# Kernel tuning notes

Hardware: AMD Instinct MI355X
Metric: run time of the kernel (lower is better)

## Reference

```python
import jax, jax.numpy as jnp
import numpy as np

T, N = 512, 256          # timesteps, parallel envs
STATE, HID = 64, 128     # input features, GRU hidden size


def setup_inputs() -> dict:
    key = jax.random.key(0)
    k = jax.random.split(key, 6)
    inputs = jax.random.normal(k[0], (T * N, STATE), dtype=jnp.float32)
    hxs = jax.random.normal(k[1], (N, HID), dtype=jnp.float32)
    masks = (jax.random.uniform(k[2], (T * N, 1)) > 0.02).astype(jnp.float32)
    # GRU params (torch layout: gates ordered r, z, n; rows = 3*HID)
    weight_ih = jax.random.normal(k[3], (3 * HID, STATE), dtype=jnp.float32) * 0.1
    weight_hh = jax.random.normal(k[4], (3 * HID, HID), dtype=jnp.float32) * 0.1
    bias_ih = jnp.zeros((3 * HID,), dtype=jnp.float32)  # init.constant_(0)
    bias_hh = jnp.zeros((3 * HID,), dtype=jnp.float32)
    return {
        "inputs": inputs, "hxs": hxs, "masks": masks,
        "weight_ih": weight_ih, "weight_hh": weight_hh,
        "bias_ih": bias_ih, "bias_hh": bias_hh,
    }


def reference(inputs, hxs, masks, weight_ih, weight_hh, bias_ih, bias_hh):
    n, hid = hxs.shape
    t = inputs.shape[0] // n
    x = inputs.reshape(t, n, -1)       # (t, n, state)
    m = masks.reshape(t, n, 1)         # (t, n, 1)

    # Input-to-gate projections are mask-independent: precompute for all steps.
    gx = jnp.einsum('tns,gs->tng', x, weight_ih) + bias_ih  # (t, n, 3H)

    def step(h, xs):
        gx_t, m_t = xs
        h = h * m_t                                 # inline reset (fused; replaces chunk splitting)
        gh = h @ weight_hh.T + bias_hh              # (n, 3H)
        xr, xz, xn = jnp.split(gx_t, 3, axis=-1)
        hr, hz, hn = jnp.split(gh, 3, axis=-1)
        r = jax.nn.sigmoid(xr + hr)
        z = jax.nn.sigmoid(xz + hz)
        cand = jnp.tanh(xn + r * hn)
        h = (1.0 - z) * cand + z * h                # torch GRU update
        return h, h

    h_final, ys = jax.lax.scan(step, hxs, (gx, m))  # ys: (t, n, H)
    return ys.reshape(t * n, hid), h_final
```

## Files before the change

kernel.cpp:

```cpp
#include <hip/hip_runtime.h>
#include <math.h>

#define T_STEPS  512
#define N_ENVS   256
#define STATE    64
#define HID      128
#define NTHREADS 512
#define XPAD     72

typedef _Float16 half8   __attribute__((ext_vector_type(8)));
typedef _Float16 half4_t __attribute__((ext_vector_type(4)));
typedef float    floatx4 __attribute__((ext_vector_type(4)));

__global__ __launch_bounds__(NTHREADS, 2) void gru_r6(
    const float* __restrict__ x,
    const float* __restrict__ h0,
    const float* __restrict__ masks,
    const float* __restrict__ wih,
    const float* __restrict__ whh,
    const float* __restrict__ bih,
    const float* __restrict__ bhh,
    float* __restrict__ out)
{
    const int b    = blockIdx.x;
    const int tid  = threadIdx.x;
    const int w    = tid >> 6;
    const int lane = tid & 63;
    const int c    = lane & 15;
    const int quad = lane >> 4;
    const int j    = 16 * w + c;

    __shared__ __align__(16) _Float16 buf[2][HID];
    __shared__ __align__(16) _Float16 xh[2][16][XPAD];
    __shared__ __align__(16) _Float16 gxp[16][HID][4];

    const int rowb[3] = { j, HID + j, 2 * HID + j };
    half8 Bh[3][4];
#pragma unroll
    for (int ti = 0; ti < 3; ++ti) {
        const int g = rowb[ti];
#pragma unroll
        for (int kt = 0; kt < 4; ++kt) {
            const float* src = whh + (size_t)g * HID + kt * 32 + quad * 8;
            const float4 p0 = *(const float4*)(src);
            const float4 p1 = *(const float4*)(src + 4);
            half8 hb;
            hb[0] = (_Float16)p0.x; hb[1] = (_Float16)p0.y;
            hb[2] = (_Float16)p0.z; hb[3] = (_Float16)p0.w;
            hb[4] = (_Float16)p1.x; hb[5] = (_Float16)p1.y;
            hb[6] = (_Float16)p1.z; hb[7] = (_Float16)p1.w;
            Bh[ti][kt] = hb;
        }
    }
    half8 Bx[3][2];
#pragma unroll
    for (int ti = 0; ti < 3; ++ti) {
        const int g = rowb[ti];
#pragma unroll
        for (int kt = 0; kt < 2; ++kt) {
            const float* src = wih + (size_t)g * STATE + kt * 32 + quad * 8;
            const float4 p0 = *(const float4*)(src);
            const float4 p1 = *(const float4*)(src + 4);
            half8 hb;
            hb[0] = (_Float16)p0.x; hb[1] = (_Float16)p0.y;
            hb[2] = (_Float16)p0.z; hb[3] = (_Float16)p0.w;
            hb[4] = (_Float16)p1.x; hb[5] = (_Float16)p1.y;
            hb[6] = (_Float16)p1.z; hb[7] = (_Float16)p1.w;
            Bx[ti][kt] = hb;
        }
    }

    const float br  = bih[j] + bhh[j];
    const float bz  = bih[HID + j] + bhh[HID + j];
    const float bxn = bih[2 * HID + j];
    const float bhn = bhh[2 * HID + j];

    float hr = h0[(size_t)b * HID + j];
    float hm = masks[b] * hr;
    if (quad == 0) buf[0][j] = (_Float16)hm;

    float4 xp = {0.f, 0.f, 0.f, 0.f};
    if (tid < 256) {
        const int k = tid >> 4, cc = (tid & 15) * 4;
        const float4 xv = *(const float4*)(x + ((size_t)k * N_ENVS + b) * STATE + cc);
        half4_t hx = {(_Float16)xv.x, (_Float16)xv.y, (_Float16)xv.z, (_Float16)xv.w};
        *(half4_t*)&xh[0][k][cc] = hx;
        xp = *(const float4*)(x + ((size_t)(16 + k) * N_ENVS + b) * STATE + cc);
    }
    float mwin  = masks[(size_t)(1  + (lane & 15)) * N_ENVS + b];
    float mwin_nxt = masks[(size_t)(17 + (lane & 15)) * N_ENVS + b];

    float o[4] = {0.f, 0.f, 0.f, 0.f};

    __syncthreads();

    const floatx4 zero4 = {0.f, 0.f, 0.f, 0.f};

    for (int tc = 0; tc < 32; ++tc) {
        if (tc > 0) {
            const int tbp = (tc - 1) * 16;
#pragma unroll
            for (int i = 0; i < 4; ++i)
                out[((size_t)(tbp + quad * 4 + i) * N_ENVS + b) * HID + j] = o[i];
            mwin = mwin_nxt;
            const int stm = (tc + 1) * 16 + 1 + (lane & 15);
            mwin_nxt = masks[(size_t)(stm < T_STEPS ? stm : T_STEPS - 1) * N_ENVS + b];
        }
        if (tid < 256) {
            const int k = tid >> 4, cc = (tid & 15) * 4;
            half4_t hx = {(_Float16)xp.x, (_Float16)xp.y, (_Float16)xp.z, (_Float16)xp.w};
            *(half4_t*)&xh[(tc + 1) & 1][k][cc] = hx;
            const int st = (tc + 2) * 16 + k;
            if (st < T_STEPS)
                xp = *(const float4*)(x + ((size_t)st * N_ENVS + b) * STATE + cc);
        }

        {
            const _Float16* xr = &xh[tc & 1][c][0];
            half8 ax0 = *(const half8*)&xr[quad * 8];
            half8 ax1 = *(const half8*)&xr[32 + quad * 8];
            floatx4 g0 = __builtin_amdgcn_mfma_f32_16x16x32_f16(ax0, Bx[0][0], zero4, 0, 0, 0);
            floatx4 g1 = __builtin_amdgcn_mfma_f32_16x16x32_f16(ax0, Bx[1][0], zero4, 0, 0, 0);
            floatx4 g2 = __builtin_amdgcn_mfma_f32_16x16x32_f16(ax0, Bx[2][0], zero4, 0, 0, 0);
            g0 = __builtin_amdgcn_mfma_f32_16x16x32_f16(ax1, Bx[0][1], g0, 0, 0, 0);
            g1 = __builtin_amdgcn_mfma_f32_16x16x32_f16(ax1, Bx[1][1], g1, 0, 0, 0);
            g2 = __builtin_amdgcn_mfma_f32_16x16x32_f16(ax1, Bx[2][1], g2, 0, 0, 0);
#pragma unroll
            for (int i = 0; i < 4; ++i) {
                half4_t p;
                p[0] = (_Float16)(g0[i] + br);
                p[1] = (_Float16)(g1[i] + bz);
                p[2] = (_Float16)(g2[i] + bxn);
                p[3] = (_Float16)0.f;
                *(half4_t*)&gxp[quad * 4 + i][j][0] = p;
            }
        }
        __syncthreads();

#pragma unroll
        for (int s = 0; s < 16; ++s) {
            const int t = tc * 16 + s;
            const _Float16* bufc = buf[s & 1];
            _Float16* bufn = (_Float16*)buf[(s + 1) & 1];

            half8 a0 = *(const half8*)(bufc + 0 * 32 + quad * 8);
            half8 a1 = *(const half8*)(bufc + 1 * 32 + quad * 8);
            half8 a2 = *(const half8*)(bufc + 2 * 32 + quad * 8);
            half8 a3 = *(const half8*)(bufc + 3 * 32 + quad * 8);
            const half4_t gxh = *(const half4_t*)&gxp[s][j][0];

            floatx4 r_a = __builtin_amdgcn_mfma_f32_16x16x32_f16(a0, Bh[0][0], zero4, 0, 0, 0);
            floatx4 r_b = __builtin_amdgcn_mfma_f32_16x16x32_f16(a2, Bh[0][2], zero4, 0, 0, 0);
            floatx4 z_a = __builtin_amdgcn_mfma_f32_16x16x32_f16(a0, Bh[1][0], zero4, 0, 0, 0);
            floatx4 z_b = __builtin_amdgcn_mfma_f32_16x16x32_f16(a2, Bh[1][2], zero4, 0, 0, 0);
            floatx4 n_a = __builtin_amdgcn_mfma_f32_16x16x32_f16(a0, Bh[2][0], zero4, 0, 0, 0);
            floatx4 n_b = __builtin_amdgcn_mfma_f32_16x16x32_f16(a2, Bh[2][2], zero4, 0, 0, 0);
            r_a = __builtin_amdgcn_mfma_f32_16x16x32_f16(a1, Bh[0][1], r_a, 0, 0, 0);
            r_b = __builtin_amdgcn_mfma_f32_16x16x32_f16(a3, Bh[0][3], r_b, 0, 0, 0);
            z_a = __builtin_amdgcn_mfma_f32_16x16x32_f16(a1, Bh[1][1], z_a, 0, 0, 0);
            z_b = __builtin_amdgcn_mfma_f32_16x16x32_f16(a3, Bh[1][3], z_b, 0, 0, 0);
            n_a = __builtin_amdgcn_mfma_f32_16x16x32_f16(a1, Bh[2][1], n_a, 0, 0, 0);
            n_b = __builtin_amdgcn_mfma_f32_16x16x32_f16(a3, Bh[2][3], n_b, 0, 0, 0);

            const float ur = (r_a[0] + r_b[0]) + (float)gxh[0];
            const float uz = (z_a[0] + z_b[0]) + (float)gxh[1];
            const float hn = (n_a[0] + n_b[0]) + bhn;
            const float xn = (float)gxh[2];

            const float e_r = __expf(-ur);
            const float r   = __builtin_amdgcn_rcpf(1.f + e_r);
            const float a   = fmaf(r, hn, xn);
            const float e_t = __expf(-2.f * fabsf(a));
            const float e_z = __expf(-fmaxf(uz, -30.f));
            const float opt = 1.f + e_t;
            float num = copysignf(e_z * (1.f - e_t), a);
            num = fmaf(hm, opt, num);
            const float den = opt * (1.f + e_z);
            const float hnew = num * __builtin_amdgcn_rcpf(den);

            o[s & 3] = (quad == (s >> 2)) ? hnew : o[s & 3];

            if (t < T_STEPS - 1) {
                const int   mi = __builtin_amdgcn_readlane(__float_as_int(mwin), s);
                const float mn = __int_as_float(mi);
                hm = mn * hnew;
                if (quad == 0) bufn[j] = (_Float16)hm;
            }
            hr = hnew;
            __syncthreads();
        }
    }

    {
        const int tbp = 31 * 16;
#pragma unroll
        for (int i = 0; i < 4; ++i)
            out[((size_t)(tbp + quad * 4 + i) * N_ENVS + b) * HID + j] = o[i];
    }
    if (quad == 0)
        out[(size_t)T_STEPS * N_ENVS * HID + (size_t)b * HID + j] = hr;
}

extern "C" void kernel_launch(void* const* d_in, const int* in_sizes, int n_in,
                              void* d_out, int out_size, void* d_ws, size_t ws_size,
                              hipStream_t stream) {
    const float* x   = (const float*)d_in[0];
    const float* h0  = (const float*)d_in[1];
    const float* mk  = (const float*)d_in[2];
    const float* wih = (const float*)d_in[3];
    const float* whh = (const float*)d_in[4];
    const float* bih = (const float*)d_in[5];
    const float* bhh = (const float*)d_in[6];
    float* out = (float*)d_out;

    hipLaunchKernelGGL(gru_r6, dim3(N_ENVS), dim3(NTHREADS), 0, stream,
                       x, h0, mk, wih, whh, bih, bhh, out);
}
```

Measured before the change: 291.9 us.

## Fold exp2 scaling into GRU weights, use raw v_exp and lighter barriers

```diff
diff --git a/kernel.cpp b/kernel.cpp
--- a/kernel.cpp
+++ b/kernel.cpp
@@ -12,7 +12,15 @@
 typedef _Float16 half4_t __attribute__((ext_vector_type(4)));
 typedef float    floatx4 __attribute__((ext_vector_type(4)));
 
-__global__ __launch_bounds__(NTHREADS, 2) void gru_r6(
+#define BAR() asm volatile("s_waitcnt lgkmcnt(0)\n\ts_barrier" ::: "memory")
+
+__device__ __forceinline__ float fexp2(float v) {
+    float r;
+    asm("v_exp_f32 %0, %1" : "=v"(r) : "v"(v));
+    return r;
+}
+
+__global__ __launch_bounds__(NTHREADS, 2) void gru_r7(
     const float* __restrict__ x,
     const float* __restrict__ h0,
     const float* __restrict__ masks,
@@ -32,23 +40,28 @@
 
     __shared__ __align__(16) _Float16 buf[2][HID];
     __shared__ __align__(16) _Float16 xh[2][16][XPAD];
-    __shared__ __align__(16) _Float16 gxp[16][HID][4];
+    __shared__ __align__(16) float    gxp[16][HID][4];
+
+    const float SRZ = -1.44269504088896341f;
+    const float SN  = -2.88539008177792681f;
+    const float scl[3] = { SRZ, SRZ, SN };
 
     const int rowb[3] = { j, HID + j, 2 * HID + j };
     half8 Bh[3][4];
 #pragma unroll
     for (int ti = 0; ti < 3; ++ti) {
         const int g = rowb[ti];
+        const float sc = scl[ti];
 #pragma unroll
         for (int kt = 0; kt < 4; ++kt) {
             const float* src = whh + (size_t)g * HID + kt * 32 + quad * 8;
             const float4 p0 = *(const float4*)(src);
             const float4 p1 = *(const float4*)(src + 4);
             half8 hb;
-            hb[0] = (_Float16)p0.x; hb[1] = (_Float16)p0.y;
-            hb[2] = (_Float16)p0.z; hb[3] = (_Float16)p0.w;
-            hb[4] = (_Float16)p1.x; hb[5] = (_Float16)p1.y;
-            hb[6] = (_Float16)p1.z; hb[7] = (_Float16)p1.w;
+            hb[0] = (_Float16)(sc * p0.x); hb[1] = (_Float16)(sc * p0.y);
+            hb[2] = (_Float16)(sc * p0.z); hb[3] = (_Float16)(sc * p0.w);
+            hb[4] = (_Float16)(sc * p1.x); hb[5] = (_Float16)(sc * p1.y);
+            hb[6] = (_Float16)(sc * p1.z); hb[7] = (_Float16)(sc * p1.w);
             Bh[ti][kt] = hb;
         }
     }
@@ -56,24 +69,25 @@
 #pragma unroll
     for (int ti = 0; ti < 3; ++ti) {
         const int g = rowb[ti];
+        const float sc = scl[ti];
 #pragma unroll
         for (int kt = 0; kt < 2; ++kt) {
             const float* src = wih + (size_t)g * STATE + kt * 32 + quad * 8;
             const float4 p0 = *(const float4*)(src);
             const float4 p1 = *(const float4*)(src + 4);
             half8 hb;
-            hb[0] = (_Float16)p0.x; hb[1] = (_Float16)p0.y;
-            hb[2] = (_Float16)p0.z; hb[3] = (_Float16)p0.w;
-            hb[4] = (_Float16)p1.x; hb[5] = (_Float16)p1.y;
-            hb[6] = (_Float16)p1.z; hb[7] = (_Float16)p1.w;
+            hb[0] = (_Float16)(sc * p0.x); hb[1] = (_Float16)(sc * p0.y);
+            hb[2] = (_Float16)(sc * p0.z); hb[3] = (_Float16)(sc * p0.w);
+            hb[4] = (_Float16)(sc * p1.x); hb[5] = (_Float16)(sc * p1.y);
+            hb[6] = (_Float16)(sc * p1.z); hb[7] = (_Float16)(sc * p1.w);
             Bx[ti][kt] = hb;
         }
     }
 
-    const float br  = bih[j] + bhh[j];
-    const float bz  = bih[HID + j] + bhh[HID + j];
-    const float bxn = bih[2 * HID + j];
-    const float bhn = bhh[2 * HID + j];
+    const float br  = SRZ * (bih[j] + bhh[j]);
+    const float bz  = SRZ * (bih[HID + j] + bhh[HID + j]);
+    const float bxn = SN  * bih[2 * HID + j];
+    const float bhn = SN  * bhh[2 * HID + j];
 
     float hr = h0[(size_t)b * HID + j];
     float hm = masks[b] * hr;
@@ -87,12 +101,12 @@
         *(half4_t*)&xh[0][k][cc] = hx;
         xp = *(const float4*)(x + ((size_t)(16 + k) * N_ENVS + b) * STATE + cc);
     }
-    float mwin  = masks[(size_t)(1  + (lane & 15)) * N_ENVS + b];
+    float mwin     = masks[(size_t)(1  + (lane & 15)) * N_ENVS + b];
     float mwin_nxt = masks[(size_t)(17 + (lane & 15)) * N_ENVS + b];
 
     float o[4] = {0.f, 0.f, 0.f, 0.f};
 
-    __syncthreads();
+    BAR();
 
     const floatx4 zero4 = {0.f, 0.f, 0.f, 0.f};
 
@@ -127,27 +141,27 @@
             g2 = __builtin_amdgcn_mfma_f32_16x16x32_f16(ax1, Bx[2][1], g2, 0, 0, 0);
 #pragma unroll
             for (int i = 0; i < 4; ++i) {
-                half4_t p;
-                p[0] = (_Float16)(g0[i] + br);
-                p[1] = (_Float16)(g1[i] + bz);
-                p[2] = (_Float16)(g2[i] + bxn);
-                p[3] = (_Float16)0.f;
-                *(half4_t*)&gxp[quad * 4 + i][j][0] = p;
+                floatx4 p;
+                p[0] = g0[i] + br;
+                p[1] = g1[i] + bz;
+                p[2] = g2[i] + bxn;
+                p[3] = 0.f;
+                *(floatx4*)&gxp[quad * 4 + i][j][0] = p;
             }
         }
-        __syncthreads();
+        BAR();
 
 #pragma unroll
         for (int s = 0; s < 16; ++s) {
-            const int t = tc * 16 + s;
             const _Float16* bufc = buf[s & 1];
             _Float16* bufn = (_Float16*)buf[(s + 1) & 1];
 
             half8 a0 = *(const half8*)(bufc + 0 * 32 + quad * 8);
+            half8 a2 = *(const half8*)(bufc + 2 * 32 + quad * 8);
             half8 a1 = *(const half8*)(bufc + 1 * 32 + quad * 8);
-            half8 a2 = *(const half8*)(bufc + 2 * 32 + quad * 8);
             half8 a3 = *(const half8*)(bufc + 3 * 32 + quad * 8);
-            const half4_t gxh = *(const half4_t*)&gxp[s][j][0];
+            const floatx4 gxh = *(const floatx4*)&gxp[s][j][0];
+            const float mn = __int_as_float(__builtin_amdgcn_readlane(__float_as_int(mwin), s));
 
             floatx4 r_a = __builtin_amdgcn_mfma_f32_16x16x32_f16(a0, Bh[0][0], zero4, 0, 0, 0);
             floatx4 r_b = __builtin_amdgcn_mfma_f32_16x16x32_f16(a2, Bh[0][2], zero4, 0, 0, 0);
@@ -162,32 +176,25 @@
             n_a = __builtin_amdgcn_mfma_f32_16x16x32_f16(a1, Bh[2][1], n_a, 0, 0, 0);
             n_b = __builtin_amdgcn_mfma_f32_16x16x32_f16(a3, Bh[2][3], n_b, 0, 0, 0);
 
-            const float ur = (r_a[0] + r_b[0]) + (float)gxh[0];
-            const float uz = (z_a[0] + z_b[0]) + (float)gxh[1];
-            const float hn = (n_a[0] + n_b[0]) + bhn;
-            const float xn = (float)gxh[2];
-
-            const float e_r = __expf(-ur);
-            const float r   = __builtin_amdgcn_rcpf(1.f + e_r);
-            const float a   = fmaf(r, hn, xn);
-            const float e_t = __expf(-2.f * fabsf(a));
-            const float e_z = __expf(-fmaxf(uz, -30.f));
+            const float urp = (r_a[0] + r_b[0]) + gxh[0];
+            const float uzp = (z_a[0] + z_b[0]) + gxh[1];
+            const float hnp = (n_a[0] + n_b[0]) + bhn;
+            const float xnp = gxh[2];
+
+            const float e_r = fexp2(urp);
+            const float rg  = __builtin_amdgcn_rcpf(1.f + e_r);
+            const float ap  = fmaf(rg, hnp, xnp);
+            const float e_t = fexp2(-fabsf(ap));
+            const float e_z = fexp2(fminf(uzp, 43.28f));
             const float opt = 1.f + e_t;
-            float num = copysignf(e_z * (1.f - e_t), a);
-            num = fmaf(hm, opt, num);
-            const float den = opt * (1.f + e_z);
-            const float hnew = num * __builtin_amdgcn_rcpf(den);
-
+            const float num = fmaf(hm, opt, -copysignf(e_z * (1.f - e_t), ap));
+            const float hnew = num * __builtin_amdgcn_rcpf(opt * (1.f + e_z));
+
+            hm = mn * hnew;
+            if (quad == 0) bufn[j] = (_Float16)hm;
             o[s & 3] = (quad == (s >> 2)) ? hnew : o[s & 3];
-
-            if (t < T_STEPS - 1) {
-                const int   mi = __builtin_amdgcn_readlane(__float_as_int(mwin), s);
-                const float mn = __int_as_float(mi);
-                hm = mn * hnew;
-                if (quad == 0) bufn[j] = (_Float16)hm;
-            }
             hr = hnew;
-            __syncthreads();
+            BAR();
         }
     }
 
@@ -213,6 +220,6 @@
     const float* bhh = (const float*)d_in[6];
     float* out = (float*)d_out;
 
-    hipLaunchKernelGGL(gru_r6, dim3(N_ENVS), dim3(NTHREADS), 0, stream,
+    hipLaunchKernelGGL(gru_r7, dim3(N_ENVS), dim3(NTHREADS), 0, stream,
                        x, h0, mk, wih, whh, bih, bhh, out);
 }
```

Result: faster. 283.4 us (-2.9%).
